# Performance work log

Measured on AMD Instinct MI355X. Metric: run time of the kernel, lower is better.

The kernel has to match this reference:

```python
import jax, jax.numpy as jnp
import numpy as np

B, S, D, H, W = 2, 8192, 512, 8, 256   # batch, seq, d_model, heads, one-sided window
HD = D // H                            # head dim = 64
C = S // W                             # number of chunks of size W (seq % 2W == 0 holds)


def setup_inputs() -> dict:
    key = jax.random.key(0)
    ks = jax.random.split(key, 7)
    x = jax.random.normal(ks[0], (B, S, D), jnp.float32)
    def w(k):
        return jax.random.normal(k, (D, D), jnp.float32) * 0.02
    def b(k):
        return jax.random.normal(k, (D,), jnp.float32) * 0.02
    return {
        "x": x,
        "Wq": w(ks[1]), "bq": b(ks[2]),
        "Wk": w(ks[3]), "bk": b(ks[4]),
        "Wv": w(ks[5]), "bv": b(ks[6]),
    }


def _heads_chunked(t):
    # (B,S,D) -> (B*H, C, W, HD): split heads, then split sequence into chunks of W
    return t.reshape(B, S, H, HD).transpose(0, 2, 1, 3).reshape(B * H, C, W, HD)


def _three_chunks(t):
    # neighbor-chunk concat: for chunk c, gather chunks [c-1, c, c+1] (zero padded at ends)
    tp = jnp.pad(t, ((0, 0), (1, 1), (0, 0), (0, 0)))
    return jnp.concatenate([tp[:, :-2], tp[:, 1:-1], tp[:, 2:]], axis=2)  # (B*H, C, 3W, HD)


def reference(x, Wq, bq, Wk, bk, Wv, bv):
    scale = 1.0 / np.sqrt(HD)
    q = _heads_chunked((x @ Wq + bq) * scale)
    k = _heads_chunked(x @ Wk + bk)
    v = _heads_chunked(x @ Wv + bv)

    k3 = _three_chunks(k)
    v3 = _three_chunks(v)

    # chunk-local scores against 3 neighboring chunks: (B*H, C, W, 3W)
    scores = jnp.einsum('bcxd,bcyd->bcxy', q, k3)

    # extract the (2W+1)-wide diagonal band: query x attends keys x..x+2W in the 3W window
    rows = jnp.arange(W)[:, None]                       # (W,1)
    diag = rows + jnp.arange(2 * W + 1)[None, :]        # (W, 2W+1) indices into 3W axis
    band = jnp.take_along_axis(scores, diag[None, None], axis=3)  # (B*H, C, W, 2W+1)

    # mask band entries whose global key position falls outside [0, S)
    pos = jnp.arange(S).reshape(C, W)[:, :, None] + (jnp.arange(2 * W + 1) - W)  # (C,W,2W+1)
    valid = (pos >= 0) & (pos < S)
    band = jnp.where(valid[None], band, -jnp.inf)

    probs = jax.nn.softmax(band, axis=-1)  # (B*H, C, W, 2W+1)

    # scatter band probs back into (W, 3W) layout and contract with values
    full = jnp.zeros((B * H, C, W, 3 * W), probs.dtype).at[:, :, rows, diag].set(probs)
    out = jnp.einsum('bcxy,bcyd->bcxd', full, v3)  # (B*H, C, W, HD)

    return out.reshape(B, H, S, HD).transpose(0, 2, 1, 3).reshape(B, S, D)
```

## Files before the change

### kernel.cpp

```cpp
#include <hip/hip_runtime.h>
#include <hip/hip_bf16.h>

#define S_LEN 8192
#define D_MODEL 512
#define NH 8
#define HD 64
#define WIN 256
#define NB 2

typedef __hip_bfloat16 bf16;
typedef __attribute__((ext_vector_type(8))) short short8;
typedef __attribute__((ext_vector_type(4))) float f32x4;

static __device__ __forceinline__ short f2bf(float f) {
    bf16 h = __float2bfloat16(f);
    return *reinterpret_cast<short*>(&h);
}

static __device__ __forceinline__ void gload_lds16(short* lds, const short* g) {
    __builtin_amdgcn_global_load_lds(
        (const __attribute__((address_space(1))) void*)g,
        (__attribute__((address_space(3))) void*)lds, 16, 0, 0);
}

__global__ __launch_bounds__(256) void convert_x_kernel(
    const float* __restrict__ x, short* __restrict__ xb)
{
    const int n4 = (NB * S_LEN * D_MODEL) / 4;
    for (int i = blockIdx.x * 256 + threadIdx.x; i < n4; i += gridDim.x * 256) {
        float4 v = ((const float4*)x)[i];
        short4 o;
        o.x = f2bf(v.x); o.y = f2bf(v.y); o.z = f2bf(v.z); o.w = f2bf(v.w);
        ((short4*)xb)[i] = o;
    }
}

__global__ __launch_bounds__(256) void convert_wT_kernel(
    const float* __restrict__ Wq, const float* __restrict__ Wk,
    const float* __restrict__ Wv, short* __restrict__ wT)
{
    __shared__ float t[32][33];
    const float* W = blockIdx.z == 0 ? Wq : (blockIdx.z == 1 ? Wk : Wv);
    const int n0 = blockIdx.x * 32, k0 = blockIdx.y * 32;
    const int tx = threadIdx.x & 31, ty = threadIdx.x >> 5;
#pragma unroll
    for (int i = 0; i < 4; ++i)
        t[ty + 8 * i][tx] = W[(size_t)(k0 + ty + 8 * i) * D_MODEL + n0 + tx];
    __syncthreads();
#pragma unroll
    for (int i = 0; i < 4; ++i) {
        const int nl = ty + 8 * i, kl = tx;
        wT[(size_t)blockIdx.z * D_MODEL * D_MODEL +
           (size_t)(n0 + nl) * D_MODEL + k0 + kl] = f2bf(t[kl][nl]);
    }
}

__global__ __launch_bounds__(256) void proj_mfma_kernel(
    const short* __restrict__ xb, const short* __restrict__ wT,
    const float* __restrict__ bq, const float* __restrict__ bk,
    const float* __restrict__ bv, bf16* __restrict__ qkv)
{
    __shared__ short Ash[128 * 64];
    __shared__ short Bsh[128 * 64];

    const int nwg  = gridDim.x * gridDim.y;
    const int orig = blockIdx.y * gridDim.x + blockIdx.x;
    const int wid  = (orig & 7) * (nwg >> 3) + (orig >> 3);
    const int bx   = wid % 12;
    const int by   = wid / 12;

    const int widx = bx >> 2;
    const int col0 = (bx & 3) * 128;
    const int row0 = by * 128;
    const int tid  = threadIdx.x;
    const int w    = tid >> 6;
    const int lane = tid & 63;
    const int col  = lane & 15;
    const int kg   = lane >> 4;

    const float* bias = widx == 0 ? bq : (widx == 1 ? bk : bv);
    const float scale = widx == 0 ? 0.125f : 1.0f;
    const short* wbase = wT + (size_t)widx * D_MODEL * D_MODEL;

    const f32x4 zero4 = {0.f, 0.f, 0.f, 0.f};
    f32x4 acc[4][4];
#pragma unroll
    for (int i = 0; i < 4; ++i)
#pragma unroll
        for (int j = 0; j < 4; ++j) acc[i][j] = zero4;

    const int wm0 = (w >> 1) * 64;
    const int wn0 = (w & 1) * 64;

    for (int kb = 0; kb < D_MODEL; kb += 64) {
#pragma unroll
        for (int ci = 0; ci < 4; ++ci) {
            const int Lb = w * 256 + ci * 64;
            const int L  = Lb + lane;
            const int m  = L >> 3;
            const int kc = ((L & 7) - (m >> 1)) & 7;
            const int ko = kb + kc * 8;
            gload_lds16(Ash + (size_t)Lb * 8,
                        xb + (size_t)(row0 + m) * D_MODEL + ko);
            gload_lds16(Bsh + (size_t)Lb * 8,
                        wbase + (size_t)(col0 + m) * D_MODEL + ko);
        }
        __syncthreads();

#pragma unroll
        for (int s = 0; s < 2; ++s) {
            short8 af[4], bfr[4];
#pragma unroll
            for (int mt = 0; mt < 4; ++mt) {
                const int m = wm0 + mt * 16 + col;
                const int c = m * 8 + ((s * 4 + kg + (m >> 1)) & 7);
                af[mt] = *(const short8*)(Ash + (size_t)c * 8);
            }
#pragma unroll
            for (int nt = 0; nt < 4; ++nt) {
                const int n = wn0 + nt * 16 + col;
                const int c = n * 8 + ((s * 4 + kg + (n >> 1)) & 7);
                bfr[nt] = *(const short8*)(Bsh + (size_t)c * 8);
            }
#pragma unroll
            for (int mt = 0; mt < 4; ++mt)
#pragma unroll
                for (int nt = 0; nt < 4; ++nt)
                    acc[mt][nt] = __builtin_amdgcn_mfma_f32_16x16x32_bf16(
                        af[mt], bfr[nt], acc[mt][nt], 0, 0, 0);
        }
        __syncthreads();
    }

    bf16* dst = qkv + (size_t)widx * (NB * NH * S_LEN * HD);
#pragma unroll
    for (int nt = 0; nt < 4; ++nt) {
        const int n = col0 + wn0 + nt * 16 + col;
        const float bias_v = bias[n];
        const int h = n >> 6, d = n & 63;
#pragma unroll
        for (int mt = 0; mt < 4; ++mt) {
            const int m0 = row0 + wm0 + mt * 16 + kg * 4;
            const int b = m0 >> 13, s0 = m0 & (S_LEN - 1);
            if (widx == 2) {
                short4 pk;
                pk.x = f2bf(acc[mt][nt][0] + bias_v);
                pk.y = f2bf(acc[mt][nt][1] + bias_v);
                pk.z = f2bf(acc[mt][nt][2] + bias_v);
                pk.w = f2bf(acc[mt][nt][3] + bias_v);
                *(short4*)&dst[(((size_t)(b * NH + h)) * HD + d) * S_LEN + s0] = pk;
            } else {
#pragma unroll
                for (int r = 0; r < 4; ++r)
                    dst[(((size_t)(b * NH + h)) * S_LEN + s0 + r) * HD + d] =
                        __float2bfloat16((acc[mt][nt][r] + bias_v) * scale);
            }
        }
    }
}

__global__ __launch_bounds__(256) void proj_kernel(
    const float* __restrict__ x, const float* __restrict__ Wm,
    const float* __restrict__ bias, bf16* __restrict__ dst, float scale,
    int transpose_v)
{
    __shared__ float As[16][64];
    __shared__ float Bs[16][64];
    const int tid  = threadIdx.x;
    const int row0 = blockIdx.y * 64;
    const int col0 = blockIdx.x * 64;
    const int ty = tid >> 4, tx = tid & 15;
    const int t4 = tid * 4;
    const int ai = t4 >> 4, aj = t4 & 15;
    const int bj = t4 >> 6, bi = t4 & 63;
    float acc[4][4] = {};
    for (int kb = 0; kb < D_MODEL; kb += 16) {
        float4 av = *(const float4*)(x  + (size_t)(row0 + ai) * D_MODEL + kb + aj);
        float4 bv = *(const float4*)(Wm + (size_t)(kb + bj)  * D_MODEL + col0 + bi);
        As[aj + 0][ai] = av.x; As[aj + 1][ai] = av.y;
        As[aj + 2][ai] = av.z; As[aj + 3][ai] = av.w;
        *(float4*)(&Bs[bj][bi]) = bv;
        __syncthreads();
#pragma unroll
        for (int k = 0; k < 16; ++k) {
            float a[4], b[4];
#pragma unroll
            for (int ii = 0; ii < 4; ++ii) a[ii] = As[k][ty * 4 + ii];
#pragma unroll
            for (int jj = 0; jj < 4; ++jj) b[jj] = Bs[k][tx * 4 + jj];
#pragma unroll
            for (int ii = 0; ii < 4; ++ii)
#pragma unroll
                for (int jj = 0; jj < 4; ++jj) acc[ii][jj] += a[ii] * b[jj];
        }
        __syncthreads();
    }
#pragma unroll
    for (int ii = 0; ii < 4; ++ii) {
        const int m = row0 + ty * 4 + ii;
        const int b = m >> 13, s = m & (S_LEN - 1);
#pragma unroll
        for (int jj = 0; jj < 4; ++jj) {
            const int n = col0 + tx * 4 + jj;
            const int h = n >> 6, d = n & 63;
            const float v = (acc[ii][jj] + bias[n]) * scale;
            if (transpose_v)
                dst[(((size_t)(b * NH + h)) * HD + d) * S_LEN + s] = __float2bfloat16(v);
            else
                dst[(((size_t)(b * NH + h)) * S_LEN + s) * HD + d] = __float2bfloat16(v);
        }
    }
}

__global__ __launch_bounds__(512) void attn_mfma5_kernel(
    const bf16* __restrict__ qw, const bf16* __restrict__ kw,
    const bf16* __restrict__ vt, float* __restrict__ out)
{
    __shared__ __align__(16) short Ksh[2][4096];
    __shared__ __align__(16) short Vsh[2][4096];
    __shared__ __align__(16) short Psh[8][16][72];

    const int orig = blockIdx.y * gridDim.x + blockIdx.x;
    const int wf   = (orig & 7) * 128 + (orig >> 3);
    const int bh   = wf >> 6;
    const int qt0  = (wf & 63) * 128;

    const int tid  = threadIdx.x;
    const int w    = tid >> 6;
    const int lane = tid & 63;
    const int col  = lane & 15;
    const int kg   = lane >> 4;
    const int q0   = qt0 + w * 16;
    const int q    = q0 + col;
    const size_t base = (size_t)bh * S_LEN * HD;

    const short* qg  = (const short*)qw;
    const short* kgp = (const short*)kw;
    const short* vgp = (const short*)vt;

    const int kt_lo = qt0 - WIN < 0 ? 0 : qt0 - WIN;
    const int kt_hi0 = qt0 + WIN + 64;
    const int kt_hi = kt_hi0 > S_LEN - 64 ? S_LEN - 64 : kt_hi0;
    const int NT    = ((kt_hi - kt_lo) >> 6) + 1;

    const int r0 = tid >> 3, c0 = (tid & 7) ^ (r0 & 7);
    const int ldsb = w * 64 * 8;

    const short* qptr = qg + base + (size_t)q * HD + kg * 8;
    const short8 qB0 = *(const short8*)(qptr);
    const short8 qB1 = *(const short8*)(qptr + 32);

    const f32x4 zero4 = {0.f, 0.f, 0.f, 0.f};
    f32x4 Oacc[4] = {zero4, zero4, zero4, zero4};
    float m = -1e30f, l = 0.f;

    const int x7 = col & 7;

    gload_lds16(&Ksh[0][ldsb], kgp + base + (size_t)(kt_lo + r0) * HD + c0 * 8);
    gload_lds16(&Vsh[0][ldsb], vgp + base + (size_t)r0 * S_LEN + kt_lo + c0 * 8);

    for (int i = 0; i < NT; ++i) {
        __syncthreads();

        if (i + 1 < NT) {
            const int ktn = kt_lo + 64 * (i + 1);
            const int nb = (i + 1) & 1;
            gload_lds16(&Ksh[nb][ldsb], kgp + base + (size_t)(ktn + r0) * HD + c0 * 8);
            gload_lds16(&Vsh[nb][ldsb], vgp + base + (size_t)r0 * S_LEN + ktn + c0 * 8);
        }

        const int kt = kt_lo + 64 * i;
        const short* Kb = Ksh[i & 1];
        const short* Vb = Vsh[i & 1];

        f32x4 sc[4];
        __builtin_amdgcn_s_setprio(1);
#pragma unroll
        for (int t = 0; t < 4; ++t) {
            const int key = 16 * t + col;
            const short8 kA0 = *(const short8*)(Kb + (size_t)(key * 8 + (kg ^ x7)) * 8);
            const short8 kA1 = *(const short8*)(Kb + (size_t)(key * 8 + ((kg + 4) ^ x7)) * 8);
            f32x4 a = zero4;
            a = __builtin_amdgcn_mfma_f32_16x16x32_bf16(kA0, qB0, a, 0, 0, 0);
            a = __builtin_amdgcn_mfma_f32_16x16x32_bf16(kA1, qB1, a, 0, 0, 0);
            sc[t] = a;
        }
        __builtin_amdgcn_s_setprio(0);

        const bool need_mask = (kt < q0 + 15 - WIN) || (kt + 63 > q0 + WIN);
        if (need_mask) {
#pragma unroll
            for (int t = 0; t < 4; ++t)
#pragma unroll
                for (int r = 0; r < 4; ++r) {
                    const int j = kt + 16 * t + kg * 4 + r;
                    if (j < q - WIN || j > q + WIN) sc[t][r] = -1e30f;
                }
        }

        float tmax = -1e30f;
#pragma unroll
        for (int t = 0; t < 4; ++t)
#pragma unroll
            for (int r = 0; r < 4; ++r) tmax = fmaxf(tmax, sc[t][r]);
        tmax = fmaxf(tmax, __shfl_xor(tmax, 16));
        tmax = fmaxf(tmax, __shfl_xor(tmax, 32));
        const float mnew = fmaxf(m, tmax);
        const float alpha = __expf(m - mnew);
        m = mnew;

        float p[4][4];
        float rs = 0.f;
        if (need_mask) {
#pragma unroll
            for (int t = 0; t < 4; ++t)
#pragma unroll
                for (int r = 0; r < 4; ++r) {
                    const float pv = (sc[t][r] > -1e29f) ? __expf(sc[t][r] - mnew) : 0.f;
                    p[t][r] = pv; rs += pv;
                }
        } else {
#pragma unroll
            for (int t = 0; t < 4; ++t)
#pragma unroll
                for (int r = 0; r < 4; ++r) {
                    const float pv = __expf(sc[t][r] - mnew);
                    p[t][r] = pv; rs += pv;
                }
        }
        rs += __shfl_xor(rs, 16);
        rs += __shfl_xor(rs, 32);
        l = l * alpha + rs;

#pragma unroll
        for (int t = 0; t < 4; ++t) {
            short4 pk;
            pk.x = f2bf(p[t][0]); pk.y = f2bf(p[t][1]);
            pk.z = f2bf(p[t][2]); pk.w = f2bf(p[t][3]);
            *(short4*)&Psh[w][col][16 * t + 4 * kg] = pk;
        }

#pragma unroll
        for (int dt = 0; dt < 4; ++dt)
#pragma unroll
            for (int r = 0; r < 4; ++r) Oacc[dt][r] *= alpha;

        const short* pp = &Psh[w][col][kg * 8];
        const short8 pB0 = *(const short8*)(pp);
        const short8 pB1 = *(const short8*)(pp + 32);

        __builtin_amdgcn_s_setprio(1);
#pragma unroll
        for (int dt = 0; dt < 4; ++dt) {
            const int d = dt * 16 + col;
            const short8 vA0 = *(const short8*)(Vb + (size_t)(d * 8 + (kg ^ x7)) * 8);
            const short8 vA1 = *(const short8*)(Vb + (size_t)(d * 8 + ((kg + 4) ^ x7)) * 8);
            Oacc[dt] = __builtin_amdgcn_mfma_f32_16x16x32_bf16(vA0, pB0, Oacc[dt], 0, 0, 0);
            Oacc[dt] = __builtin_amdgcn_mfma_f32_16x16x32_bf16(vA1, pB1, Oacc[dt], 0, 0, 0);
        }
        __builtin_amdgcn_s_setprio(0);
    }

    const float inv = 1.0f / l;
    const int b = bh >> 3, h = bh & 7;
    float* op = out + ((size_t)(b * S_LEN + q)) * D_MODEL + h * HD + kg * 4;
#pragma unroll
    for (int dt = 0; dt < 4; ++dt) {
        float4 o;
        o.x = Oacc[dt][0] * inv; o.y = Oacc[dt][1] * inv;
        o.z = Oacc[dt][2] * inv; o.w = Oacc[dt][3] * inv;
        *(float4*)(op + dt * 16) = o;
    }
}

extern "C" void kernel_launch(void* const* d_in, const int* in_sizes, int n_in,
                              void* d_out, int out_size, void* d_ws, size_t ws_size,
                              hipStream_t stream)
{
    const float* x  = (const float*)d_in[0];
    const float* Wq = (const float*)d_in[1];
    const float* bq = (const float*)d_in[2];
    const float* Wk = (const float*)d_in[3];
    const float* bk = (const float*)d_in[4];
    const float* Wv = (const float*)d_in[5];
    const float* bv = (const float*)d_in[6];
    float* out = (float*)d_out;

    const size_t n_elem = (size_t)NB * NH * S_LEN * HD;
    bf16* qw = (bf16*)d_ws;
    bf16* kw = qw + n_elem;
    bf16* vw = kw + n_elem;
    short* xb = (short*)(vw + n_elem);
    short* wT = xb + (size_t)NB * S_LEN * D_MODEL;

    const size_t need = (3 * n_elem + (size_t)NB * S_LEN * D_MODEL +
                         3 * (size_t)D_MODEL * D_MODEL) * sizeof(short);

    if (ws_size >= need) {
        convert_x_kernel<<<2048, 256, 0, stream>>>(x, xb);
        dim3 wgrid(D_MODEL / 32, D_MODEL / 32, 3);
        convert_wT_kernel<<<wgrid, 256, 0, stream>>>(Wq, Wk, Wv, wT);
        dim3 ggrid(12, (NB * S_LEN) / 128);
        proj_mfma_kernel<<<ggrid, 256, 0, stream>>>(xb, wT, bq, bk, bv, qw);
    } else {
        dim3 pgrid(D_MODEL / 64, (NB * S_LEN) / 64);
        proj_kernel<<<pgrid, 256, 0, stream>>>(x, Wq, bq, qw, 0.125f, 0);
        proj_kernel<<<pgrid, 256, 0, stream>>>(x, Wk, bk, kw, 1.0f, 0);
        proj_kernel<<<pgrid, 256, 0, stream>>>(x, Wv, bv, vw, 1.0f, 1);
    }

    dim3 agrid(NB * NH, S_LEN / 128);
    attn_mfma5_kernel<<<agrid, 512, 0, stream>>>(qw, kw, vw, out);
}
```

Baseline: 179.3 us.

## Use exp2 softmax with lazy rescaling and per-warp window tile skipping

Folds log2(e) into the Q projection scale so the softmax uses exp2f directly. Rescaling of the output accumulator and running sum happens only when the running max grows by more than a threshold, reducing per-tile multiply work. Each warp now skips key tiles entirely outside its own query window, and the max/sum reductions are tree-structured. Lazy rescaling relies on bounded score growth and could risk precision if scores vary widely.

```diff
diff --git a/kernel.cpp b/kernel.cpp
--- a/kernel.cpp
+++ b/kernel.cpp
@@ -7,6 +7,8 @@
 #define HD 64
 #define WIN 256
 #define NB 2
+
+#define QSCALE 0.1803368801111204f
 
 typedef __hip_bfloat16 bf16;
 typedef __attribute__((ext_vector_type(8))) short short8;
@@ -79,7 +81,7 @@
     const int kg   = lane >> 4;
 
     const float* bias = widx == 0 ? bq : (widx == 1 ? bk : bv);
-    const float scale = widx == 0 ? 0.125f : 1.0f;
+    const float scale = widx == 0 ? QSCALE : 1.0f;
     const short* wbase = wT + (size_t)widx * D_MODEL * D_MODEL;
 
     const f32x4 zero4 = {0.f, 0.f, 0.f, 0.f};
@@ -243,6 +245,9 @@
     const int kt_hi = kt_hi0 > S_LEN - 64 ? S_LEN - 64 : kt_hi0;
     const int NT    = ((kt_hi - kt_lo) >> 6) + 1;
 
+    const int wlo = q0 - WIN;
+    const int whi = q0 + 15 + WIN;
+
     const int r0 = tid >> 3, c0 = (tid & 7) ^ (r0 & 7);
     const int ldsb = w * 64 * 8;
 
@@ -270,6 +275,8 @@
         }
 
         const int kt = kt_lo + 64 * i;
+        if (kt + 63 < wlo || kt > whi) continue;
+
         const short* Kb = Ksh[i & 1];
         const short* Vb = Vsh[i & 1];
 
@@ -298,39 +305,39 @@
                 }
         }
 
-        float tmax = -1e30f;
-#pragma unroll
-        for (int t = 0; t < 4; ++t)
-#pragma unroll
-            for (int r = 0; r < 4; ++r) tmax = fmaxf(tmax, sc[t][r]);
+        float tm0 = fmaxf(fmaxf(sc[0][0], sc[0][1]), fmaxf(sc[0][2], sc[0][3]));
+        float tm1 = fmaxf(fmaxf(sc[1][0], sc[1][1]), fmaxf(sc[1][2], sc[1][3]));
+        float tm2 = fmaxf(fmaxf(sc[2][0], sc[2][1]), fmaxf(sc[2][2], sc[2][3]));
+        float tm3 = fmaxf(fmaxf(sc[3][0], sc[3][1]), fmaxf(sc[3][2], sc[3][3]));
+        float tmax = fmaxf(fmaxf(tm0, tm1), fmaxf(tm2, tm3));
         tmax = fmaxf(tmax, __shfl_xor(tmax, 16));
         tmax = fmaxf(tmax, __shfl_xor(tmax, 32));
-        const float mnew = fmaxf(m, tmax);
-        const float alpha = __expf(m - mnew);
-        m = mnew;
+
+        if (__any(tmax > m + 8.f)) {
+            const float mnew = fmaxf(m, tmax);
+            const float alpha = exp2f(m - mnew);
+            m = mnew;
+#pragma unroll
+            for (int dt = 0; dt < 4; ++dt)
+#pragma unroll
+                for (int r = 0; r < 4; ++r) Oacc[dt][r] *= alpha;
+            l *= alpha;
+        }
 
         float p[4][4];
-        float rs = 0.f;
-        if (need_mask) {
-#pragma unroll
-            for (int t = 0; t < 4; ++t)
-#pragma unroll
-                for (int r = 0; r < 4; ++r) {
-                    const float pv = (sc[t][r] > -1e29f) ? __expf(sc[t][r] - mnew) : 0.f;
-                    p[t][r] = pv; rs += pv;
-                }
-        } else {
-#pragma unroll
-            for (int t = 0; t < 4; ++t)
-#pragma unroll
-                for (int r = 0; r < 4; ++r) {
-                    const float pv = __expf(sc[t][r] - mnew);
-                    p[t][r] = pv; rs += pv;
-                }
-        }
+#pragma unroll
+        for (int t = 0; t < 4; ++t)
+#pragma unroll
+            for (int r = 0; r < 4; ++r) p[t][r] = exp2f(sc[t][r] - m);
+
+        float r0s = (p[0][0] + p[0][1]) + (p[0][2] + p[0][3]);
+        float r1s = (p[1][0] + p[1][1]) + (p[1][2] + p[1][3]);
+        float r2s = (p[2][0] + p[2][1]) + (p[2][2] + p[2][3]);
+        float r3s = (p[3][0] + p[3][1]) + (p[3][2] + p[3][3]);
+        float rs = (r0s + r1s) + (r2s + r3s);
         rs += __shfl_xor(rs, 16);
         rs += __shfl_xor(rs, 32);
-        l = l * alpha + rs;
+        l += rs;
 
 #pragma unroll
         for (int t = 0; t < 4; ++t) {
@@ -339,11 +346,6 @@
             pk.z = f2bf(p[t][2]); pk.w = f2bf(p[t][3]);
             *(short4*)&Psh[w][col][16 * t + 4 * kg] = pk;
         }
-
-#pragma unroll
-        for (int dt = 0; dt < 4; ++dt)
-#pragma unroll
-            for (int r = 0; r < 4; ++r) Oacc[dt][r] *= alpha;
 
         const short* pp = &Psh[w][col][kg * 8];
         const short8 pB0 = *(const short8*)(pp);
@@ -404,7 +406,7 @@
         proj_mfma_kernel<<<ggrid, 256, 0, stream>>>(xb, wT, bq, bk, bv, qw);
     } else {
         dim3 pgrid(D_MODEL / 64, (NB * S_LEN) / 64);
-        proj_kernel<<<pgrid, 256, 0, stream>>>(x, Wq, bq, qw, 0.125f, 0);
+        proj_kernel<<<pgrid, 256, 0, stream>>>(x, Wq, bq, qw, QSCALE, 0);
         proj_kernel<<<pgrid, 256, 0, stream>>>(x, Wk, bk, kw, 1.0f, 0);
         proj_kernel<<<pgrid, 256, 0, stream>>>(x, Wv, bv, vw, 1.0f, 1);
     }
```

New measurement: 180.8 us. No clear change (+0.8%).
